# Kernel tuning notes

Hardware: AMD Instinct MI355X
Metric: run time of the kernel (lower is better)

The kernel has to match this reference:

```python
import jax, jax.numpy as jnp
import numpy as np

NEG = -1e8


def lstm_scan(x, lens, Wih, Whh, b):
    # x: [B,S,D], lens: [B] int. PyTorch gate order i,f,g,o. Returns [B,S,H], zero at pad.
    B, S, D = x.shape
    H = Whh.shape[1]
    xs = jnp.swapaxes(x, 0, 1)  # [S,B,D]
    ts = jnp.arange(S)

    def step(carry, inp):
        h, c = carry
        xt, t = inp
        gates = xt @ Wih.T + h @ Whh.T + b  # [B,4H]
        i, f, g, o = jnp.split(gates, 4, axis=-1)
        i, f, o = jax.nn.sigmoid(i), jax.nn.sigmoid(f), jax.nn.sigmoid(o)
        g = jnp.tanh(g)
        c_new = f * c + i * g
        h_new = o * jnp.tanh(c_new)
        valid = (t < lens)[:, None]
        h = jnp.where(valid, h_new, h)
        c = jnp.where(valid, c_new, c)
        out = jnp.where(valid, h_new, 0.0)
        return (h, c), out

    init = (jnp.zeros((B, H), x.dtype), jnp.zeros((B, H), x.dtype))
    _, outs = jax.lax.scan(step, init, (xs, ts))
    return jnp.swapaxes(outs, 0, 1)  # [B,S,H]


def bilstm(x, lens, Wih_f, Whh_f, b_f, Wih_b, Whh_b, b_b):
    # forward direction
    out_f = lstm_scan(x, lens, Wih_f, Whh_f, b_f)
    # backward: reverse the valid prefix per sample (packed-sequence semantics)
    S = x.shape[1]
    t = jnp.arange(S)[None, :]
    idx = jnp.where(t < lens[:, None], lens[:, None] - 1 - t, t)  # [B,S]
    xr = jnp.take_along_axis(x, idx[:, :, None], axis=1)
    out_r = lstm_scan(xr, lens, Wih_b, Whh_b, b_b)
    out_b = jnp.take_along_axis(out_r, idx[:, :, None], axis=1)
    return jnp.concatenate([out_f, out_b], axis=-1)


def tnet_forward(seqs_id, seqs_len, asps_len, asps_mask, sent_mask,
                 embed, Wih_f, Whh_f, b_f, Wih_b, Whh_b, b_b,
                 W_cpt, b_cpt, W_as, b_as, Wq, bq, Wk, bk, Wv, bv, Wd, bd):
    seqs = embed[seqs_id]                                   # [B,S,D] (dropout = eval identity)
    seqs_lstm = bilstm(seqs, seqs_len, Wih_f, Whh_f, b_f, Wih_b, Whh_b, b_b)  # [B,S,D]

    # ragged aspect gather + pad + mean == masked mean (asps_mask==0 marks aspect tokens)
    asp_sel = (asps_mask == 0).astype(seqs_lstm.dtype)       # [B,S]
    asps = (seqs_lstm * asp_sel[:, :, None]).sum(axis=1) / asps_len[:, None].astype(seqs_lstm.dtype)
    asps = asps[:, None, :]                                  # [B,1,D]

    # CPT layers (flag='AS'); Attentions = dot-product attn, out = softmax(QK^T + mask) @ K
    x = seqs_lstm
    for _ in range(2):
        score = jax.nn.softmax(jnp.einsum('bqd,bkd->bqk', x, seqs_lstm) + asps_mask[:, None, :], axis=-1)
        attn_out = jnp.einsum('bqk,bkd->bqd', score, seqs_lstm)
        combine = jnp.concatenate([attn_out, x], axis=-1)    # [B,S,2D]
        linear_out = jax.nn.relu(combine @ W_cpt.T + b_cpt)
        scale = jax.nn.sigmoid(x @ W_as.T + b_as)
        x = scale * linear_out + (1.0 - scale) * x

    # QKVAttention over sentence
    D = x.shape[-1]
    Qp = asps @ Wq.T + bq                                    # [B,1,D]
    Kp = x @ Wk.T + bk                                       # [B,S,D]
    Vp = x @ Wv.T + bv
    sc = jax.nn.softmax(jnp.einsum('bqd,bkd->bqk', Qp, Kp) / jnp.sqrt(jnp.asarray(D, x.dtype))
                        + sent_mask[:, None, :], axis=-1)    # [B,1,S]
    out = jnp.einsum('bqk,bkd->bqd', sc, Vp)                 # [B,1,D]
    logits = out[:, 0] @ Wd.T + bd                           # [B,n_class]
    return logits, sc[:, 0]


def setup_inputs() -> dict:
    B, S, V, D, H, NC = 64, 256, 30000, 512, 256, 3
    key = jax.random.key(0)
    ks = jax.random.split(key, 24)

    seqs_id = jax.random.randint(ks[0], (B, S), 0, V)
    seqs_len = jax.random.randint(ks[1], (B,), S // 2, S + 1)
    asps_len = jax.random.randint(ks[2], (B,), 1, 6)
    start = jax.random.randint(ks[3], (B,), 0, S // 2 - 8)   # aspect span inside valid prefix
    pos = jnp.arange(S)[None, :]
    in_span = (pos >= start[:, None]) & (pos < (start + asps_len)[:, None])
    asps_mask = jnp.where(in_span, 0.0, NEG).astype(jnp.float32)
    sent_mask = jnp.where(pos < seqs_len[:, None], 0.0, NEG).astype(jnp.float32)

    def nrm(k, shape, s=0.02):
        return (s * jax.random.normal(k, shape)).astype(jnp.float32)

    inp = dict(seqs_id=seqs_id, seqs_len=seqs_len, asps_len=asps_len,
               asps_mask=asps_mask, sent_mask=sent_mask,
               embed=nrm(ks[4], (V, D), 0.1),
               Wih_f=nrm(ks[5], (4 * H, D)), Whh_f=nrm(ks[6], (4 * H, H)), b_f=jnp.zeros((4 * H,), jnp.float32),
               Wih_b=nrm(ks[7], (4 * H, D)), Whh_b=nrm(ks[8], (4 * H, H)), b_b=jnp.zeros((4 * H,), jnp.float32),
               W_cpt=nrm(ks[9], (D, 2 * D)), b_cpt=jnp.zeros((D,), jnp.float32),
               W_as=nrm(ks[10], (D, D)), b_as=jnp.zeros((D,), jnp.float32),
               Wq=nrm(ks[11], (D, D)), bq=jnp.zeros((D,), jnp.float32),
               Wk=nrm(ks[12], (D, D)), bk=jnp.zeros((D,), jnp.float32),
               Wv=nrm(ks[13], (D, D)), bv=jnp.zeros((D,), jnp.float32),
               Wd=nrm(ks[14], (NC, D)), bd=jnp.zeros((NC,), jnp.float32))
    return inp


def reference(seqs_id, seqs_len, asps_len, asps_mask, sent_mask,
              embed, Wih_f, Whh_f, b_f, Wih_b, Whh_b, b_b,
              W_cpt, b_cpt, W_as, b_as, Wq, bq, Wk, bk, Wv, bv, Wd, bd):
    return tnet_forward(seqs_id, seqs_len, asps_len, asps_mask, sent_mask,
                        embed, Wih_f, Whh_f, b_f, Wih_b, Whh_b, b_b,
                        W_cpt, b_cpt, W_as, b_as, Wq, bq, Wk, bk, Wv, bv, Wd, bd)
```

## Files before the change

kernel.cpp:

```cpp
#include <hip/hip_runtime.h>
#include <math.h>

constexpr int B_ = 64, S_ = 256, D_ = 512, H_ = 256, NC_ = 3;
constexpr int BS = B_ * S_;
constexpr int G4 = 4 * H_;

typedef __attribute__((ext_vector_type(4))) float f32x4;
typedef __attribute__((ext_vector_type(8))) short s16x8;
typedef unsigned short u16;
typedef unsigned long long u64;

template<int ACT>
static __device__ __forceinline__ float activate(float v) {
  if constexpr (ACT == 1) return v > 0.f ? v : 0.f;
  else if constexpr (ACT == 2) return 1.f / (1.f + expf(-v));
  else return v;
}

static __device__ __forceinline__ u16 f2bf_rne(float f) {
  unsigned u = __float_as_uint(f);
  return (u16)((u + 0x7FFFu + ((u >> 16) & 1u)) >> 16);
}
static __device__ __forceinline__ float bf2f(u16 h) {
  return __uint_as_float(((unsigned)h) << 16);
}
static __device__ __forceinline__ void splitf(float f, u16& h, u16& l) {
  h = f2bf_rne(f);
  float r = f - bf2f(h);
  l = f2bf_rne(r);
}

__global__ __launch_bounds__(256) void split_w(
    const float* __restrict__ src, u16* __restrict__ h, u16* __restrict__ l, int n4)
{
  int i = blockIdx.x * 256 + threadIdx.x;
  if (i >= n4) return;
  float4 v = ((const float4*)src)[i];
  ushort4 hh, ll;
  splitf(v.x, hh.x, ll.x); splitf(v.y, hh.y, ll.y);
  splitf(v.z, hh.z, ll.z); splitf(v.w, hh.w, ll.w);
  ((ushort4*)h)[i] = hh;
  ((ushort4*)l)[i] = ll;
}

__global__ __launch_bounds__(256) void gather_split(
    const float* __restrict__ embed, const int* __restrict__ gidx,
    u16* __restrict__ h, u16* __restrict__ l)
{
  int i = blockIdx.x * 256 + threadIdx.x;
  if (i >= BS * D_ / 4) return;
  int r = i >> 7;
  int c = (i & 127) << 2;
  float4 v = *(const float4*)(embed + (size_t)gidx[r] * D_ + c);
  ushort4 hh, ll;
  splitf(v.x, hh.x, ll.x); splitf(v.y, hh.y, ll.y);
  splitf(v.z, hh.z, ll.z); splitf(v.w, hh.w, ll.w);
  ((ushort4*)h)[i] = hh;
  ((ushort4*)l)[i] = ll;
}

template<int ACT, bool BT, bool ADDC, bool ASPL, bool BSPL, bool OSPL>
__global__ __launch_bounds__(256) void mgemm(
    const float* __restrict__ Af, const u16* __restrict__ Ah, const u16* __restrict__ Al,
    const float* __restrict__ Bf, const u16* __restrict__ Bh, const u16* __restrict__ Bl,
    const float* __restrict__ bias, const float* __restrict__ Cin,
    float* __restrict__ Co, u16* __restrict__ Oh, u16* __restrict__ Ol,
    int M, int N, int K, int ldb, long sA, long sB, long sC)
{
  __shared__ u16 AH[128][40];
  __shared__ u16 AL[128][40];
  __shared__ u16 BH[128][40];
  __shared__ u16 BL[128][40];

  const int tid = threadIdx.x;
  const int w = tid >> 6, l = tid & 63;
  const int m0 = blockIdx.x * 128, n0 = blockIdx.y * 128;
  const long zA = (long)blockIdx.z * sA;
  const long zB = (long)blockIdx.z * sB;
  const long zC = (long)blockIdx.z * sC;

  f32x4 acc[2][8];
  #pragma unroll
  for (int i = 0; i < 2; ++i)
    #pragma unroll
    for (int j = 0; j < 8; ++j) acc[i][j] = (f32x4){0.f, 0.f, 0.f, 0.f};

  const int ar = tid >> 1, ahh = tid & 1;
  const int bk = tid >> 3, bnq = tid & 7;
  const int lr = l & 15, lk = (l >> 4) * 8;

  for (int kt = 0; kt < K; kt += 32) {
    {
      int m = m0 + ar;
      if constexpr (ASPL) {
        s16x8 h0 = (s16x8)0, h1 = (s16x8)0, l0 = (s16x8)0, l1 = (s16x8)0;
        if (m < M) {
          const u16* ph = Ah + zA + (size_t)m * K + kt + ahh * 16;
          const u16* pl = Al + zA + (size_t)m * K + kt + ahh * 16;
          h0 = *(const s16x8*)ph; h1 = *(const s16x8*)(ph + 8);
          l0 = *(const s16x8*)pl; l1 = *(const s16x8*)(pl + 8);
        }
        *(s16x8*)&AH[ar][ahh * 16] = h0; *(s16x8*)&AH[ar][ahh * 16 + 8] = h1;
        *(s16x8*)&AL[ar][ahh * 16] = l0; *(s16x8*)&AL[ar][ahh * 16 + 8] = l1;
      } else {
        float vv[16];
        if (m < M) {
          const float* pf = Af + zA + (size_t)m * K + kt + ahh * 16;
          #pragma unroll
          for (int c = 0; c < 4; ++c) {
            float4 v = ((const float4*)pf)[c];
            vv[c * 4] = v.x; vv[c * 4 + 1] = v.y; vv[c * 4 + 2] = v.z; vv[c * 4 + 3] = v.w;
          }
        } else {
          #pragma unroll
          for (int c = 0; c < 16; ++c) vv[c] = 0.f;
        }
        u16 hh[16], ll[16];
        #pragma unroll
        for (int c = 0; c < 16; ++c) splitf(vv[c], hh[c], ll[c]);
        *(s16x8*)&AH[ar][ahh * 16] = *(s16x8*)&hh[0];
        *(s16x8*)&AH[ar][ahh * 16 + 8] = *(s16x8*)&hh[8];
        *(s16x8*)&AL[ar][ahh * 16] = *(s16x8*)&ll[0];
        *(s16x8*)&AL[ar][ahh * 16 + 8] = *(s16x8*)&ll[8];
      }
    }
    if constexpr (BT) {
      if constexpr (BSPL) {
        const u16* ph = Bh + zB + (size_t)(n0 + ar) * ldb + kt + ahh * 16;
        const u16* pl = Bl + zB + (size_t)(n0 + ar) * ldb + kt + ahh * 16;
        *(s16x8*)&BH[ar][ahh * 16] = *(const s16x8*)ph;
        *(s16x8*)&BH[ar][ahh * 16 + 8] = *(const s16x8*)(ph + 8);
        *(s16x8*)&BL[ar][ahh * 16] = *(const s16x8*)pl;
        *(s16x8*)&BL[ar][ahh * 16 + 8] = *(const s16x8*)(pl + 8);
      } else {
        const float* pf = Bf + zB + (size_t)(n0 + ar) * ldb + kt + ahh * 16;
        float vv[16];
        #pragma unroll
        for (int c = 0; c < 4; ++c) {
          float4 v = ((const float4*)pf)[c];
          vv[c * 4] = v.x; vv[c * 4 + 1] = v.y; vv[c * 4 + 2] = v.z; vv[c * 4 + 3] = v.w;
        }
        u16 hh[16], ll[16];
        #pragma unroll
        for (int c = 0; c < 16; ++c) splitf(vv[c], hh[c], ll[c]);
        *(s16x8*)&BH[ar][ahh * 16] = *(s16x8*)&hh[0];
        *(s16x8*)&BH[ar][ahh * 16 + 8] = *(s16x8*)&hh[8];
        *(s16x8*)&BL[ar][ahh * 16] = *(s16x8*)&ll[0];
        *(s16x8*)&BL[ar][ahh * 16 + 8] = *(s16x8*)&ll[8];
      }
    } else {
      const u16* ph = Bh + zB + (size_t)(kt + bk) * ldb + n0 + bnq * 16;
      const u16* pl = Bl + zB + (size_t)(kt + bk) * ldb + n0 + bnq * 16;
      s16x8 h8a = *(const s16x8*)ph, h8b = *(const s16x8*)(ph + 8);
      s16x8 l8a = *(const s16x8*)pl, l8b = *(const s16x8*)(pl + 8);
      #pragma unroll
      for (int jj = 0; jj < 8; ++jj) {
        BH[bnq * 16 + jj][bk] = (u16)h8a[jj];
        BH[bnq * 16 + 8 + jj][bk] = (u16)h8b[jj];
        BL[bnq * 16 + jj][bk] = (u16)l8a[jj];
        BL[bnq * 16 + 8 + jj][bk] = (u16)l8b[jj];
      }
    }
    __syncthreads();

    s16x8 afh[2], afl[2];
    #pragma unroll
    for (int i = 0; i < 2; ++i) {
      afh[i] = *(const s16x8*)&AH[w * 32 + i * 16 + lr][lk];
      afl[i] = *(const s16x8*)&AL[w * 32 + i * 16 + lr][lk];
    }
    #pragma unroll
    for (int j = 0; j < 8; ++j) {
      s16x8 bfh = *(const s16x8*)&BH[j * 16 + lr][lk];
      s16x8 bfl = *(const s16x8*)&BL[j * 16 + lr][lk];
      #pragma unroll
      for (int i = 0; i < 2; ++i) {
        acc[i][j] = __builtin_amdgcn_mfma_f32_16x16x32_bf16(afl[i], bfh, acc[i][j], 0, 0, 0);
        acc[i][j] = __builtin_amdgcn_mfma_f32_16x16x32_bf16(afh[i], bfl, acc[i][j], 0, 0, 0);
        acc[i][j] = __builtin_amdgcn_mfma_f32_16x16x32_bf16(afh[i], bfh, acc[i][j], 0, 0, 0);
      }
    }
    __syncthreads();
  }

  const int rl = (l >> 4) * 4;
  #pragma unroll
  for (int j = 0; j < 8; ++j) {
    int n = n0 + j * 16 + lr;
    float bv = bias ? bias[n] : 0.f;
    #pragma unroll
    for (int i = 0; i < 2; ++i) {
      #pragma unroll
      for (int e = 0; e < 4; ++e) {
        int m = m0 + w * 32 + i * 16 + rl + e;
        if (m < M) {
          float v = acc[i][j][e] + bv;
          if constexpr (ADDC) v += Cin[zC + (size_t)m * N + n];
          v = activate<ACT>(v);
          if constexpr (OSPL) {
            u16 hh, ll; splitf(v, hh, ll);
            Oh[zC + (size_t)m * N + n] = hh;
            Ol[zC + (size_t)m * N + n] = ll;
          } else {
            Co[zC + (size_t)m * N + n] = v;
          }
        }
      }
    }
  }
}

__global__ __launch_bounds__(256) void wf_prep(
    const float* __restrict__ Wf, const float* __restrict__ Wb, u16* __restrict__ WF)
{
  int gid = blockIdx.x * 256 + threadIdx.x;
  int lane = gid & 63;
  int nt = (gid >> 6) & 1;
  int kt = (gid >> 7) & 7;
  int w  = (gid >> 10) & 3;
  int j  = (gid >> 12) & 7;
  int dir = gid >> 15;
  const float* W = dir ? Wb : Wf;
  int r = w * 256 + j * 32 + nt * 16 + (lane & 15);
  int kb = kt * 32 + (lane >> 4) * 8;
  const float* src = W + (size_t)r * H_ + kb;
  u16 hh[8], ll[8];
  #pragma unroll
  for (int c = 0; c < 2; ++c) {
    float4 v = ((const float4*)src)[c];
    splitf(v.x, hh[c*4+0], ll[c*4+0]); splitf(v.y, hh[c*4+1], ll[c*4+1]);
    splitf(v.z, hh[c*4+2], ll[c*4+2]); splitf(v.w, hh[c*4+3], ll[c*4+3]);
  }
  size_t off = (size_t)(gid >> 6) * 1024 + (size_t)lane * 8;
  *(s16x8*)(WF + off)       = *(s16x8*)&hh[0];
  *(s16x8*)(WF + off + 512) = *(s16x8*)&ll[0];
}

__global__ __launch_bounds__(256) void ring_init(u64* __restrict__ ring64)
{
  int i = blockIdx.x * 256 + threadIdx.x;
  __hip_atomic_store(&ring64[i], (u64)3, __ATOMIC_RELAXED, __HIP_MEMORY_SCOPE_AGENT);
}

__global__ __launch_bounds__(256, 1) void lstm_dist(
    const float* __restrict__ GX, const u16* __restrict__ WF,
    const int* __restrict__ lens, u16* __restrict__ outH, u16* __restrict__ outL,
    u64* __restrict__ ring64)
{
  const int bid = blockIdx.x;
  const int grp = bid & 7;
  const int j   = bid >> 3;
  const int dir = grp >> 2;
  const int bg  = grp & 3;
  const int b0g = bg * 16;
  const int tid = threadIdx.x;
  const int w = tid >> 6, l = tid & 63;

  const float* gx = GX + (size_t)dir * ((size_t)BS * G4);

  __shared__ int slen[16];
  __shared__ __align__(16) u16 AHs[16][264];
  __shared__ __align__(16) u16 ALs[16][264];
  __shared__ float act[2][4][16][33];
  if (tid < 16) slen[tid] = lens[b0g + tid];
  __syncthreads();

  s16x8 wh[8][2], wl[8][2];
  #pragma unroll
  for (int kt = 0; kt < 8; ++kt)
    #pragma unroll
    for (int nt = 0; nt < 2; ++nt) {
      size_t q = ((size_t)(((dir * 8 + j) * 4 + w) * 8 + kt) * 2 + nt);
      const u16* p = WF + q * 1024 + (size_t)l * 8;
      wh[kt][nt] = *(const s16x8*)p;
      wl[kt][nt] = *(const s16x8*)(p + 512);
    }

  const int ub = tid >> 4;
  const int uu = (tid & 15) * 2;
  const int len_b = slen[ub];
  float c0s = 0.f, c1s = 0.f, h0s = 0.f, h1s = 0.f;

  const int lr = l & 15, lkb = (l >> 4) * 8;

  for (int t = 0; t < S_; ++t) {
    float gxv[2][4];
    #pragma unroll
    for (int nt = 0; nt < 2; ++nt)
      #pragma unroll
      for (int e = 0; e < 4; ++e) {
        int b = (l >> 4) * 4 + e;
        int len = slen[b];
        int pos = dir ? (t < len ? len - 1 - t : t) : t;
        gxv[nt][e] = gx[(size_t)((b0g + b) * S_ + pos) * G4 + (w * 256 + j * 32 + nt * 16 + lr)];
      }

    f32x4 acc[2];
    acc[0] = (f32x4){0.f, 0.f, 0.f, 0.f};
    acc[1] = (f32x4){0.f, 0.f, 0.f, 0.f};

    if (t > 0) {
      const unsigned gen = (unsigned)(((t - 1) >> 2) & 3);
      const int slot = (t - 1) & 3;
      u64* rb = ring64 + ((size_t)slot * 8 + grp) * (16 * 128);
      u64 v[8];
      unsigned need = 0xFFu;
      do {
        unsigned nn = 0;
        #pragma unroll
        for (int k = 0; k < 8; ++k)
          if ((need >> k) & 1)
            v[k] = __hip_atomic_load(&rb[k * 256 + tid], __ATOMIC_RELAXED, __HIP_MEMORY_SCOPE_AGENT);
        #pragma unroll
        for (int k = 0; k < 8; ++k)
          if (((need >> k) & 1) && ((unsigned)v[k] & 3u) != gen) nn |= 1u << k;
        need = nn;
      } while (need);
      #pragma unroll
      for (int k = 0; k < 8; ++k) {
        int idx = k * 256 + tid;
        int b = idx >> 7, p = idx & 127;
        float f0 = __uint_as_float((unsigned)v[k] & ~3u);
        float f1 = __uint_as_float((unsigned)(v[k] >> 32));
        u16 hh0, ll0, hh1, ll1;
        splitf(f0, hh0, ll0); splitf(f1, hh1, ll1);
        *(unsigned*)&AHs[b][2 * p] = (unsigned)hh0 | ((unsigned)hh1 << 16);
        *(unsigned*)&ALs[b][2 * p] = (unsigned)ll0 | ((unsigned)ll1 << 16);
      }
      __syncthreads();
      #pragma unroll
      for (int kt = 0; kt < 8; ++kt) {
        s16x8 ah = *(const s16x8*)&AHs[lr][kt * 32 + lkb];
        s16x8 al = *(const s16x8*)&ALs[lr][kt * 32 + lkb];
        #pragma unroll
        for (int nt = 0; nt < 2; ++nt) {
          acc[nt] = __builtin_amdgcn_mfma_f32_16x16x32_bf16(al, wh[kt][nt], acc[nt], 0, 0, 0);
          acc[nt] = __builtin_amdgcn_mfma_f32_16x16x32_bf16(ah, wl[kt][nt], acc[nt], 0, 0, 0);
          acc[nt] = __builtin_amdgcn_mfma_f32_16x16x32_bf16(ah, wh[kt][nt], acc[nt], 0, 0, 0);
        }
      }
    }

    const int pb = t & 1;
    #pragma unroll
    for (int nt = 0; nt < 2; ++nt)
      #pragma unroll
      for (int e = 0; e < 4; ++e) {
        float v = acc[nt][e] + gxv[nt][e];
        v = (w == 2) ? tanhf(v) : 1.f / (1.f + expf(-v));
        act[pb][w][(l >> 4) * 4 + e][nt * 16 + lr] = v;
      }
    __syncthreads();

    {
      int pos = dir ? (t < len_b ? len_b - 1 - t : t) : t;
      bool valid = t < len_b;
      float i0 = act[pb][0][ub][uu],     f0 = act[pb][1][ub][uu],     g0 = act[pb][2][ub][uu],     o0 = act[pb][3][ub][uu];
      float i1 = act[pb][0][ub][uu + 1], f1 = act[pb][1][ub][uu + 1], g1 = act[pb][2][ub][uu + 1], o1 = act[pb][3][ub][uu + 1];
      float cn0 = fmaf(f0, c0s, i0 * g0), cn1 = fmaf(f1, c1s, i1 * g1);
      float hn0 = o0 * tanhf(cn0), hn1 = o1 * tanhf(cn1);
      if (valid) { c0s = cn0; h0s = hn0; c1s = cn1; h1s = hn1; }
      unsigned gen = (unsigned)((t >> 2) & 3);
      unsigned a0 = (__float_as_uint(h0s) & ~3u) | gen;
      unsigned a1 = __float_as_uint(h1s);
      u64 word = ((u64)a1 << 32) | (u64)a0;
      const int slot = t & 3;
      size_t ridx = ((size_t)slot * 8 + grp) * (16 * 128) + (size_t)ub * 128 + j * 16 + (tid & 15);
      __hip_atomic_store(&ring64[ridx], word, __ATOMIC_RELAXED, __HIP_MEMORY_SCOPE_AGENT);
      float ov0 = valid ? hn0 : 0.f, ov1 = valid ? hn1 : 0.f;
      u16 oh0, qq0, oh1, qq1;
      splitf(ov0, oh0, qq0); splitf(ov1, oh1, qq1);
      size_t obase = (size_t)((b0g + ub) * S_ + pos) * (2 * H_) + dir * H_ + j * 32 + uu;
      *(ushort2*)&outH[obase] = make_ushort2(oh0, oh1);
      *(ushort2*)&outL[obase] = make_ushort2(qq0, qq1);
    }
  }
}

__global__ __launch_bounds__(512) void asps_k(
    const u16* __restrict__ lh, const u16* __restrict__ ll,
    const float* __restrict__ amask, const int* __restrict__ alen, float* __restrict__ asps)
{
  int b = blockIdx.x, tid = threadIdx.x;
  __shared__ int sstart;
  if (tid == 0) sstart = S_;
  __syncthreads();
  if (tid < S_ && amask[b * S_ + tid] == 0.f) atomicMin(&sstart, tid);
  __syncthreads();
  const int start = sstart;
  const int len = alen[b];
  float acc = 0.f;
  for (int k = 0; k < len; ++k) {
    size_t i = ((size_t)(b * S_ + start + k)) * D_ + tid;
    acc += bf2f(lh[i]) + bf2f(ll[i]);
  }
  asps[b * D_ + tid] = acc / (float)len;
}

__global__ __launch_bounds__(256) void softmax_rows(
    const float* __restrict__ p_, const float* __restrict__ mask,
    u16* __restrict__ ph, u16* __restrict__ pl)
{
  const int row = blockIdx.x;
  const int b = row >> 8;
  const int tid = threadIdx.x;
  const float* p = p_ + (size_t)row * S_;
  float v = p[tid] + mask[(b << 8) | tid];
  float m = v;
  #pragma unroll
  for (int off = 32; off > 0; off >>= 1) m = fmaxf(m, __shfl_xor(m, off));
  __shared__ float r1[4];
  __shared__ float r2[4];
  const int w = tid >> 6, l = tid & 63;
  if (l == 0) r1[w] = m;
  __syncthreads();
  m = fmaxf(fmaxf(r1[0], r1[1]), fmaxf(r1[2], r1[3]));
  float e = expf(v - m);
  float s = e;
  #pragma unroll
  for (int off = 32; off > 0; off >>= 1) s += __shfl_xor(s, off);
  if (l == 0) r2[w] = s;
  __syncthreads();
  s = r2[0] + r2[1] + r2[2] + r2[3];
  float o = e / s;
  u16 hh, ll; splitf(o, hh, ll);
  ph[(size_t)row * S_ + tid] = hh;
  pl[(size_t)row * S_ + tid] = ll;
}

__global__ __launch_bounds__(256) void xupdate(
    const u16* __restrict__ xh, const u16* __restrict__ xl,
    const float4* __restrict__ sc, const float4* __restrict__ lin,
    u16* __restrict__ oh, u16* __restrict__ ol, int n4)
{
  int i = blockIdx.x * 256 + threadIdx.x;
  if (i >= n4) return;
  ushort4 h4 = ((const ushort4*)xh)[i];
  ushort4 l4 = ((const ushort4*)xl)[i];
  float4 s = sc[i], lv = lin[i];
  float x0 = bf2f(h4.x) + bf2f(l4.x);
  float x1 = bf2f(h4.y) + bf2f(l4.y);
  float x2 = bf2f(h4.z) + bf2f(l4.z);
  float x3 = bf2f(h4.w) + bf2f(l4.w);
  float o0 = s.x * lv.x + (1.f - s.x) * x0;
  float o1 = s.y * lv.y + (1.f - s.y) * x1;
  float o2 = s.z * lv.z + (1.f - s.z) * x2;
  float o3 = s.w * lv.w + (1.f - s.w) * x3;
  ushort4 hh, ll;
  splitf(o0, hh.x, ll.x); splitf(o1, hh.y, ll.y);
  splitf(o2, hh.z, ll.z); splitf(o3, hh.w, ll.w);
  ((ushort4*)oh)[i] = hh;
  ((ushort4*)ol)[i] = ll;
}

__global__ __launch_bounds__(256) void final_sc_k(
    const float* __restrict__ Qp, const float* __restrict__ Kp,
    const float* __restrict__ smask, float* __restrict__ outsc)
{
  int b = blockIdx.x, tid = threadIdx.x;
  __shared__ float q[D_];
  q[tid] = Qp[b * D_ + tid];
  q[tid + 256] = Qp[b * D_ + tid + 256];
  __syncthreads();
  const float4* kr = (const float4*)(Kp + ((size_t)(b * S_ + tid)) * D_);
  float acc = 0.f;
  #pragma unroll 4
  for (int d = 0; d < D_ / 4; ++d) {
    float4 kv = kr[d];
    acc += q[4 * d] * kv.x + q[4 * d + 1] * kv.y + q[4 * d + 2] * kv.z + q[4 * d + 3] * kv.w;
  }
  float v = acc / sqrtf((float)D_) + smask[b * S_ + tid];
  float m = v;
  #pragma unroll
  for (int off = 32; off > 0; off >>= 1) m = fmaxf(m, __shfl_xor(m, off));
  __shared__ float r1[4];
  __shared__ float r2[4];
  const int w = tid >> 6, l = tid & 63;
  if (l == 0) r1[w] = m;
  __syncthreads();
  m = fmaxf(fmaxf(r1[0], r1[1]), fmaxf(r1[2], r1[3]));
  float e = expf(v - m);
  float s = e;
  #pragma unroll
  for (int off = 32; off > 0; off >>= 1) s += __shfl_xor(s, off);
  if (l == 0) r2[w] = s;
  __syncthreads();
  s = r2[0] + r2[1] + r2[2] + r2[3];
  outsc[b * S_ + tid] = e / s;
}

__global__ __launch_bounds__(512) void zero_outv(float* __restrict__ p)
{
  p[blockIdx.x * 512 + threadIdx.x] = 0.f;
}

__global__ __launch_bounds__(512) void out_vec_k(
    const float* __restrict__ sc, const float* __restrict__ Vp, float* __restrict__ outv)
{
  int b = blockIdx.x, d = threadIdx.x;
  int k0 = blockIdx.y * 32;
  __shared__ float s[32];
  if (d < 32) s[d] = sc[b * S_ + k0 + d];
  __syncthreads();
  float acc = 0.f;
  #pragma unroll
  for (int k = 0; k < 32; ++k)
    acc = fmaf(s[k], Vp[((size_t)(b * S_ + k0 + k)) * D_ + d], acc);
  atomicAdd(&outv[b * D_ + d], acc);
}

__global__ __launch_bounds__(192) void logits_k(
    const float* __restrict__ outv, const float* __restrict__ Wd,
    const float* __restrict__ bd, float* __restrict__ out)
{
  int b = blockIdx.x;
  int c = threadIdx.x >> 6, l = threadIdx.x & 63;
  float acc = 0.f;
  for (int d = l; d < D_; d += 64) acc = fmaf(outv[b * D_ + d], Wd[c * D_ + d], acc);
  #pragma unroll
  for (int off = 32; off > 0; off >>= 1) acc += __shfl_down(acc, off);
  if (l == 0) out[b * NC_ + c] = acc + bd[c];
}

extern "C" void kernel_launch(void* const* d_in, const int* in_sizes, int n_in,
                              void* d_out, int out_size, void* d_ws, size_t ws_size,
                              hipStream_t stream)
{
  const int*   seqs_id   = (const int*)d_in[0];
  const int*   seqs_len  = (const int*)d_in[1];
  const int*   asps_len  = (const int*)d_in[2];
  const float* asps_mask = (const float*)d_in[3];
  const float* sent_mask = (const float*)d_in[4];
  const float* embed     = (const float*)d_in[5];
  const float* Wih_f     = (const float*)d_in[6];
  const float* Whh_f     = (const float*)d_in[7];
  const float* b_f       = (const float*)d_in[8];
  const float* Wih_b     = (const float*)d_in[9];
  const float* Whh_b     = (const float*)d_in[10];
  const float* b_b       = (const float*)d_in[11];
  const float* W_cpt     = (const float*)d_in[12];
  const float* b_cpt     = (const float*)d_in[13];
  const float* W_as      = (const float*)d_in[14];
  const float* b_as      = (const float*)d_in[15];
  const float* Wq        = (const float*)d_in[16];
  const float* bq        = (const float*)d_in[17];
  const float* Wk        = (const float*)d_in[18];
  const float* bk        = (const float*)d_in[19];
  const float* Wv        = (const float*)d_in[20];
  const float* bv        = (const float*)d_in[21];
  const float* Wd        = (const float*)d_in[22];
  const float* bd        = (const float*)d_in[23];

  float* w = (float*)d_ws;
  size_t off = 0;
  auto alloc = [&](size_t words) { size_t o = off; off += words; return o; };
  struct Split { u16* h; u16* l; };
  auto salloc = [&](size_t n) {
    size_t o = alloc(n);
    Split s; s.h = (u16*)(w + o); s.l = (u16*)(w + o) + n; return s;
  };

  const size_t off_wf   = alloc(524288);
  const size_t off_ring = alloc(131072);
  Split sWihF = salloc(4ul * H_ * D_);
  Split sWihB = salloc(4ul * H_ * D_);
  Split sWcpt = salloc((size_t)D_ * 2 * D_);
  Split sWas  = salloc((size_t)D_ * D_);
  Split sWk   = salloc((size_t)D_ * D_);
  Split sWv   = salloc((size_t)D_ * D_);
  Split sWq   = salloc((size_t)D_ * D_);
  Split sLstm = salloc((size_t)BS * D_);
  const size_t off_asps = alloc((size_t)B_ * D_);
  const size_t off_qp   = alloc((size_t)B_ * D_);
  const size_t off_outv = alloc((size_t)B_ * D_);

  const size_t dyn0 = off;
  Split sXemb; sXemb.h = (u16*)(w + dyn0); sXemb.l = sXemb.h + (size_t)BS * D_;
  float* GX = w + dyn0 + (size_t)BS * D_;
  size_t p2 = dyn0;
  float* scoreF = w + p2;                 p2 += (size_t)B_ * S_ * S_;
  Split sScore; sScore.h = (u16*)(w + p2); sScore.l = sScore.h + (size_t)B_ * S_ * S_; p2 += (size_t)B_ * S_ * S_;
  Split sAttn;  sAttn.h  = (u16*)(w + p2); sAttn.l  = sAttn.h + (size_t)BS * D_;       p2 += (size_t)BS * D_;
  float* lin = w + p2;                    p2 += (size_t)BS * D_;
  float* scl = w + p2;                    p2 += (size_t)BS * D_;
  Split sX;     sX.h     = (u16*)(w + p2); sX.l     = sX.h + (size_t)BS * D_;           p2 += (size_t)BS * D_;

  u16* WF      = (u16*)(w + off_wf);
  u64* ring64  = (u64*)(w + off_ring);
  float* aspsb = w + off_asps;
  float* qp    = w + off_qp;
  float* outv  = w + off_outv;
  float* Kp    = (float*)sAttn.h;
  float* Vp    = lin;
  float* logits = (float*)d_out;
  float* outsc  = (float*)d_out + B_ * NC_;

  ring_init<<<256, 256, 0, stream>>>(ring64);
  wf_prep<<<256, 256, 0, stream>>>(Whh_f, Whh_b, WF);
  split_w<<<512, 256, 0, stream>>>(Wih_f, sWihF.h, sWihF.l, H_ * D_);
  split_w<<<512, 256, 0, stream>>>(Wih_b, sWihB.h, sWihB.l, H_ * D_);
  split_w<<<512, 256, 0, stream>>>(W_cpt, sWcpt.h, sWcpt.l, D_ * 2 * D_ / 4);
  split_w<<<256, 256, 0, stream>>>(W_as, sWas.h, sWas.l, D_ * D_ / 4);
  split_w<<<256, 256, 0, stream>>>(Wk, sWk.h, sWk.l, D_ * D_ / 4);
  split_w<<<256, 256, 0, stream>>>(Wv, sWv.h, sWv.l, D_ * D_ / 4);
  split_w<<<256, 256, 0, stream>>>(Wq, sWq.h, sWq.l, D_ * D_ / 4);
  gather_split<<<BS * D_ / 4 / 256, 256, 0, stream>>>(embed, seqs_id, sXemb.h, sXemb.l);

  mgemm<0, true, false, true, true, false><<<dim3(128, 8, 1), 256, 0, stream>>>(
      nullptr, sXemb.h, sXemb.l, nullptr, sWihF.h, sWihF.l, b_f, nullptr,
      GX, nullptr, nullptr, BS, G4, D_, D_, 0, 0, 0);
  mgemm<0, true, false, true, true, false><<<dim3(128, 8, 1), 256, 0, stream>>>(
      nullptr, sXemb.h, sXemb.l, nullptr, sWihB.h, sWihB.l, b_b, nullptr,
      GX + (size_t)BS * G4, nullptr, nullptr, BS, G4, D_, D_, 0, 0, 0);

  lstm_dist<<<64, 256, 0, stream>>>(GX, WF, seqs_len, sLstm.h, sLstm.l, ring64);
  asps_k<<<B_, 512, 0, stream>>>(sLstm.h, sLstm.l, asps_mask, asps_len, aspsb);

  for (int it = 0; it < 2; ++it) {
    const Split xin = (it == 0) ? sLstm : sX;
    mgemm<0, true, false, true, true, false><<<dim3(2, 2, B_), 256, 0, stream>>>(
        nullptr, xin.h, xin.l, nullptr, sLstm.h, sLstm.l, nullptr, nullptr,
        scoreF, nullptr, nullptr, S_, S_, D_, D_,
        (long)S_ * D_, (long)S_ * D_, (long)S_ * S_);
    softmax_rows<<<BS, 256, 0, stream>>>(scoreF, asps_mask, sScore.h, sScore.l);
    mgemm<0, false, false, true, true, true><<<dim3(2, 4, B_), 256, 0, stream>>>(
        nullptr, sScore.h, sScore.l, nullptr, sLstm.h, sLstm.l, nullptr, nullptr,
        nullptr, sAttn.h, sAttn.l, S_, D_, S_, D_,
        (long)S_ * S_, (long)S_ * D_, (long)S_ * D_);
    mgemm<0, true, false, true, true, false><<<dim3(128, 4, 1), 256, 0, stream>>>(
        nullptr, sAttn.h, sAttn.l, nullptr, sWcpt.h, sWcpt.l, b_cpt, nullptr,
        lin, nullptr, nullptr, BS, D_, D_, 2 * D_, 0, 0, 0);
    mgemm<1, true, true, true, true, false><<<dim3(128, 4, 1), 256, 0, stream>>>(
        nullptr, xin.h, xin.l, nullptr, sWcpt.h + D_, sWcpt.l + D_, nullptr, lin,
        lin, nullptr, nullptr, BS, D_, D_, 2 * D_, 0, 0, 0);
    mgemm<2, true, false, true, true, false><<<dim3(128, 4, 1), 256, 0, stream>>>(
        nullptr, xin.h, xin.l, nullptr, sWas.h, sWas.l, b_as, nullptr,
        scl, nullptr, nullptr, BS, D_, D_, D_, 0, 0, 0);
    xupdate<<<(BS * D_ / 4 + 255) / 256, 256, 0, stream>>>(
        xin.h, xin.l, (const float4*)scl, (const float4*)lin, sX.h, sX.l, BS * D_ / 4);
  }

  mgemm<0, true, false, true, true, false><<<dim3(128, 4, 1), 256, 0, stream>>>(
      nullptr, sX.h, sX.l, nullptr, sWk.h, sWk.l, bk, nullptr,
      Kp, nullptr, nullptr, BS, D_, D_, D_, 0, 0, 0);
  mgemm<0, true, false, true, true, false><<<dim3(128, 4, 1), 256, 0, stream>>>(
      nullptr, sX.h, sX.l, nullptr, sWv.h, sWv.l, bv, nullptr,
      Vp, nullptr, nullptr, BS, D_, D_, D_, 0, 0, 0);
  mgemm<0, true, false, false, true, false><<<dim3(1, 4, 1), 256, 0, stream>>>(
      aspsb, nullptr, nullptr, nullptr, sWq.h, sWq.l, bq, nullptr,
      qp, nullptr, nullptr, B_, D_, D_, D_, 0, 0, 0);

  zero_outv<<<B_ * D_ / 512, 512, 0, stream>>>(outv);
  final_sc_k<<<B_, 256, 0, stream>>>(qp, Kp, sent_mask, outsc);
  out_vec_k<<<dim3(B_, 8, 1), 512, 0, stream>>>(outsc, Vp, outv);
  logits_k<<<B_, 192, 0, stream>>>(outv, Wd, bd, logits);
}
```

Before: 1.556 ms.

## Add fast-path mirror ring with inline-asm sc0 loads for LSTM step exchange

Each recurrent step now writes the hidden-state word to a second mirror ring with a plain volatile store, alongside the relaxed agent-scope atomic store. Readers first poll the mirror with a batch of eight inline-asm sc0 loads and a single waitcnt, retrying up to four times, and fall back to the original atomic polling loop only if needed. Both halves of each 64-bit word now carry generation tags, so a torn or partial write is detected. The aim is to cut cross-block synchronization latency on the serial recurrence, at the cost of extra store traffic and reliance on cache-coherence behaviour of sc0 loads. The ring_init launch is doubled so it also initializes the mirror ring, which is allocated immediately after the original ring.

```diff
diff --git a/kernel.cpp b/kernel.cpp
--- a/kernel.cpp
+++ b/kernel.cpp
@@ -239,13 +239,14 @@
 __global__ __launch_bounds__(256) void ring_init(u64* __restrict__ ring64)
 {
   int i = blockIdx.x * 256 + threadIdx.x;
-  __hip_atomic_store(&ring64[i], (u64)3, __ATOMIC_RELAXED, __HIP_MEMORY_SCOPE_AGENT);
+  __hip_atomic_store(&ring64[i], 0x0000000300000003ULL,
+                     __ATOMIC_RELAXED, __HIP_MEMORY_SCOPE_AGENT);
 }
 
 __global__ __launch_bounds__(256, 1) void lstm_dist(
     const float* __restrict__ GX, const u16* __restrict__ WF,
     const int* __restrict__ lens, u16* __restrict__ outH, u16* __restrict__ outL,
-    u64* __restrict__ ring64)
+    u64* __restrict__ ring64, u64* __restrict__ ringF)
 {
   const int bid = blockIdx.x;
   const int grp = bid & 7;
@@ -302,26 +303,65 @@
     if (t > 0) {
       const unsigned gen = (unsigned)(((t - 1) >> 2) & 3);
       const int slot = (t - 1) & 3;
-      u64* rb = ring64 + ((size_t)slot * 8 + grp) * (16 * 128);
+      const size_t rbase = ((size_t)slot * 8 + grp) * (16 * 128);
+      u64* rb = ring64 + rbase;
+      const u64* rf = ringF + rbase;
       u64 v[8];
-      unsigned need = 0xFFu;
-      do {
-        unsigned nn = 0;
+      const u64* q0 = rf + 0 * 256 + tid;
+      const u64* q1 = rf + 1 * 256 + tid;
+      const u64* q2 = rf + 2 * 256 + tid;
+      const u64* q3 = rf + 3 * 256 + tid;
+      const u64* q4 = rf + 4 * 256 + tid;
+      const u64* q5 = rf + 5 * 256 + tid;
+      const u64* q6 = rf + 6 * 256 + tid;
+      const u64* q7 = rf + 7 * 256 + tid;
+      bool got = false;
+      for (int tryi = 0; tryi < 4 && !got; ++tryi) {
+        asm volatile(
+          "global_load_dwordx2 %0, %8, off sc0\n\t"
+          "global_load_dwordx2 %1, %9, off sc0\n\t"
+          "global_load_dwordx2 %2, %10, off sc0\n\t"
+          "global_load_dwordx2 %3, %11, off sc0\n\t"
+          "global_load_dwordx2 %4, %12, off sc0\n\t"
+          "global_load_dwordx2 %5, %13, off sc0\n\t"
+          "global_load_dwordx2 %6, %14, off sc0\n\t"
+          "global_load_dwordx2 %7, %15, off sc0\n\t"
+          "s_waitcnt vmcnt(0)"
+          : "=&v"(v[0]), "=&v"(v[1]), "=&v"(v[2]), "=&v"(v[3]),
+            "=&v"(v[4]), "=&v"(v[5]), "=&v"(v[6]), "=&v"(v[7])
+          : "v"(q0), "v"(q1), "v"(q2), "v"(q3),
+            "v"(q4), "v"(q5), "v"(q6), "v"(q7)
+          : "memory");
+        unsigned bad = 0;
         #pragma unroll
-        for (int k = 0; k < 8; ++k)
-          if ((need >> k) & 1)
-            v[k] = __hip_atomic_load(&rb[k * 256 + tid], __ATOMIC_RELAXED, __HIP_MEMORY_SCOPE_AGENT);
-        #pragma unroll
-        for (int k = 0; k < 8; ++k)
-          if (((need >> k) & 1) && ((unsigned)v[k] & 3u) != gen) nn |= 1u << k;
-        need = nn;
-      } while (need);
+        for (int k = 0; k < 8; ++k) {
+          bad |= ((unsigned)v[k] & 3u) ^ gen;
+          bad |= ((unsigned)(v[k] >> 32) & 3u) ^ gen;
+        }
+        got = (bad == 0);
+      }
+      if (!got) {
+        unsigned need = 0xFFu;
+        do {
+          unsigned nn = 0;
+          #pragma unroll
+          for (int k = 0; k < 8; ++k)
+            if ((need >> k) & 1)
+              v[k] = __hip_atomic_load(&rb[k * 256 + tid], __ATOMIC_RELAXED, __HIP_MEMORY_SCOPE_AGENT);
+          #pragma unroll
+          for (int k = 0; k < 8; ++k)
+            if (((need >> k) & 1) &&
+                ((((unsigned)v[k] & 3u) != gen) || (((unsigned)(v[k] >> 32) & 3u) != gen)))
+              nn |= 1u << k;
+          need = nn;
+        } while (need);
+      }
       #pragma unroll
       for (int k = 0; k < 8; ++k) {
         int idx = k * 256 + tid;
         int b = idx >> 7, p = idx & 127;
         float f0 = __uint_as_float((unsigned)v[k] & ~3u);
-        float f1 = __uint_as_float((unsigned)(v[k] >> 32));
+        float f1 = __uint_as_float((unsigned)(v[k] >> 32) & ~3u);
         u16 hh0, ll0, hh1, ll1;
         splitf(f0, hh0, ll0); splitf(f1, hh1, ll1);
         *(unsigned*)&AHs[b][2 * p] = (unsigned)hh0 | ((unsigned)hh1 << 16);
@@ -362,10 +402,11 @@
       if (valid) { c0s = cn0; h0s = hn0; c1s = cn1; h1s = hn1; }
       unsigned gen = (unsigned)((t >> 2) & 3);
       unsigned a0 = (__float_as_uint(h0s) & ~3u) | gen;
-      unsigned a1 = __float_as_uint(h1s);
+      unsigned a1 = (__float_as_uint(h1s) & ~3u) | gen;
       u64 word = ((u64)a1 << 32) | (u64)a0;
       const int slot = t & 3;
       size_t ridx = ((size_t)slot * 8 + grp) * (16 * 128) + (size_t)ub * 128 + j * 16 + (tid & 15);
+      *(volatile u64*)&ringF[ridx] = word;
       __hip_atomic_store(&ring64[ridx], word, __ATOMIC_RELAXED, __HIP_MEMORY_SCOPE_AGENT);
       float ov0 = valid ? hn0 : 0.f, ov1 = valid ? hn1 : 0.f;
       u16 oh0, qq0, oh1, qq1;
@@ -560,8 +601,9 @@
     Split s; s.h = (u16*)(w + o); s.l = (u16*)(w + o) + n; return s;
   };
 
-  const size_t off_wf   = alloc(524288);
-  const size_t off_ring = alloc(131072);
+  const size_t off_wf    = alloc(524288);
+  const size_t off_ring  = alloc(131072);
+  const size_t off_ringf = alloc(131072);
   Split sWihF = salloc(4ul * H_ * D_);
   Split sWihB = salloc(4ul * H_ * D_);
   Split sWcpt = salloc((size_t)D_ * 2 * D_);
@@ -587,6 +629,7 @@
 
   u16* WF      = (u16*)(w + off_wf);
   u64* ring64  = (u64*)(w + off_ring);
+  u64* ringF   = (u64*)(w + off_ringf);
   float* aspsb = w + off_asps;
   float* qp    = w + off_qp;
   float* outv  = w + off_outv;
@@ -595,7 +638,7 @@
   float* logits = (float*)d_out;
   float* outsc  = (float*)d_out + B_ * NC_;
 
-  ring_init<<<256, 256, 0, stream>>>(ring64);
+  ring_init<<<512, 256, 0, stream>>>(ring64);
   wf_prep<<<256, 256, 0, stream>>>(Whh_f, Whh_b, WF);
   split_w<<<512, 256, 0, stream>>>(Wih_f, sWihF.h, sWihF.l, H_ * D_);
   split_w<<<512, 256, 0, stream>>>(Wih_b, sWihB.h, sWihB.l, H_ * D_);
@@ -613,7 +656,7 @@
       nullptr, sXemb.h, sXemb.l, nullptr, sWihB.h, sWihB.l, b_b, nullptr,
       GX + (size_t)BS * G4, nullptr, nullptr, BS, G4, D_, D_, 0, 0, 0);
 
-  lstm_dist<<<64, 256, 0, stream>>>(GX, WF, seqs_len, sLstm.h, sLstm.l, ring64);
+  lstm_dist<<<64, 256, 0, stream>>>(GX, WF, seqs_len, sLstm.h, sLstm.l, ring64, ringF);
   asps_k<<<B_, 512, 0, stream>>>(sLstm.h, sLstm.l, asps_mask, asps_len, aspsb);
 
   for (int it = 0; it < 2; ++it) {
```

Result: slower. 1.714 ms (+10.2%).
